# Kernel optimization log

Measured on AMD Instinct MI355X. Metric: run time of the kernel, lower is better.

The kernel has to match this reference:

```python
import jax, jax.numpy as jnp
import numpy as np

N_NODES = 50000
N_EDGES = 400000
EMB_DIM = 256
N_LAYERS = 5
MAX_NODES = 50          # nodes per graph (equal-size graphs)
N_GRAPHS = N_NODES // MAX_NODES
BN_EPS = 1e-5


def setup_inputs() -> dict:
    key = jax.random.key(0)
    ks = jax.random.split(key, 12)
    D = EMB_DIM
    x = jax.random.normal(ks[0], (N_NODES, D), dtype=jnp.float32)
    edge_index = jax.random.randint(ks[1], (2, N_EDGES), 0, N_NODES, dtype=jnp.int64)
    edge_attr = jax.random.randint(ks[2], (N_EDGES, 2), 0, 3, dtype=jnp.int64)
    batch = (jnp.arange(N_NODES, dtype=jnp.int64) // MAX_NODES)
    # per-layer parameters, stacked on leading layer axis
    s1 = 1.0 / np.sqrt(D)
    s2 = 1.0 / np.sqrt(2 * D)
    W1 = jax.random.uniform(ks[3], (N_LAYERS, D, 2 * D), jnp.float32, -s1, s1)
    b1 = jax.random.uniform(ks[4], (N_LAYERS, 2 * D), jnp.float32, -s1, s1)
    W2 = jax.random.uniform(ks[5], (N_LAYERS, 2 * D, D), jnp.float32, -s2, s2)
    b2 = jax.random.uniform(ks[6], (N_LAYERS, D), jnp.float32, -s2, s2)
    # xavier_uniform for edge embeddings
    g1 = np.sqrt(6.0 / (6 + D))
    g2 = np.sqrt(6.0 / (3 + D))
    E1 = jax.random.uniform(ks[7], (N_LAYERS, 6, D), jnp.float32, -g1, g1)
    E2 = jax.random.uniform(ks[8], (N_LAYERS, 3, D), jnp.float32, -g2, g2)
    gamma = jnp.ones((N_LAYERS, D), jnp.float32)
    beta = jnp.zeros((N_LAYERS, D), jnp.float32)
    return {"x": x, "edge_index": edge_index, "edge_attr": edge_attr,
            "batch": batch, "W1": W1, "b1": b1, "W2": W2, "b2": b2,
            "E1": E1, "E2": E2, "gamma": gamma, "beta": beta}


def reference(x, edge_index, edge_attr, batch, W1, b1, W2, b2, E1, E2, gamma, beta):
    N, D = x.shape
    # add self loops once (edge_index/edge_attr are identical every layer);
    # self-loop edge_attr fill_value = 0
    loop = jnp.arange(N, dtype=edge_index.dtype)
    src = jnp.concatenate([edge_index[0], loop])
    dst = jnp.concatenate([edge_index[1], loop])
    ea0 = jnp.concatenate([edge_attr[:, 0], jnp.zeros((N,), edge_attr.dtype)])
    ea1 = jnp.concatenate([edge_attr[:, 1], jnp.zeros((N,), edge_attr.dtype)])

    h = x
    L = W1.shape[0]
    for l in range(L):
        # GINConv: message = x_j + edge_embedding, aggr='add', update = MLP
        eemb = E1[l][ea0] + E2[l][ea1]                       # [E+N, D]
        msg = h[src] + eemb                                   # gather + add
        agg = jax.ops.segment_sum(msg, dst, num_segments=N)   # scatter-add
        h = jnp.maximum(agg @ W1[l] + b1[l], 0.0) @ W2[l] + b2[l]
        # BatchNorm1d (training mode: batch statistics over nodes)
        mu = h.mean(axis=0)
        var = h.var(axis=0)
        h = (h - mu) / jnp.sqrt(var + BN_EPS) * gamma[l] + beta[l]
        if l < L - 1:
            h = jnp.maximum(h, 0.0)  # relu (dropout p=0 is identity)

    # pad_sequence over graphs: scatter node reps into [G, MAX_NODES, D]
    G = N // MAX_NODES
    ones = jnp.ones((N,), jnp.int32)
    counts = jax.ops.segment_sum(ones, batch, num_segments=G)
    starts = jnp.cumsum(counts) - counts
    pos = jnp.arange(N) - starts[batch]
    padded = jnp.zeros((G, MAX_NODES, D), h.dtype).at[batch, pos].set(h)
    return padded
```

## Files before the change

kernel.cpp:

```cpp
#include <hip/hip_runtime.h>

#define NN 50000
#define NE 400000
#define DIM 256
#define HID 512
#define NL 5
#define BN_EPS 1e-5f
#define NB_SCAN 196

typedef float float4v __attribute__((ext_vector_type(4)));
typedef _Float16 half8 __attribute__((ext_vector_type(8)));
typedef _Float16 half4v __attribute__((ext_vector_type(4)));

__device__ __forceinline__ void gl_lds16(const void* g, void* l) {
    __builtin_amdgcn_global_load_lds((__attribute__((address_space(1))) void*)g,
                                     (__attribute__((address_space(3))) void*)l, 16, 0, 0);
}


__global__ void k_zero(int* p, int n) {
    int i = blockIdx.x * blockDim.x + threadIdx.x;
    if (i < n) p[i] = 0;
}

__global__ void k_x2h(const float* __restrict__ x, _Float16* __restrict__ xh) {
    int i = blockIdx.x * blockDim.x + threadIdx.x;
    if (i >= NN * DIM / 4) return;
    float4 v = ((const float4*)x)[i];
    half4v o;
    o.x = (_Float16)v.x; o.y = (_Float16)v.y; o.z = (_Float16)v.z; o.w = (_Float16)v.w;
    ((half4v*)xh)[i] = o;
}

__global__ void k_ctab(const float* __restrict__ E1, const float* __restrict__ E2,
                       float* __restrict__ C) {
    int b = blockIdx.x;
    int l = b / 9, ab = b % 9;
    int a = ab / 3, bb = ab % 3;
    int c = threadIdx.x;
    C[(size_t)b * DIM + c] = E1[(size_t)(l * 6 + a) * DIM + c] + E2[(size_t)(l * 3 + bb) * DIM + c];
}

__global__ void k_hist(const int* __restrict__ ei, int* __restrict__ counts) {
    int e = blockIdx.x * blockDim.x + threadIdx.x;
    if (e < NE) atomicAdd(&counts[ei[NE + e]], 1);
}

__global__ void k_bsum(const int* __restrict__ counts, int* __restrict__ bsum) {
    __shared__ int s[256];
    int t = threadIdx.x;
    int i = blockIdx.x * 256 + t;
    s[t] = (i < NN) ? counts[i] : 0;
    __syncthreads();
    for (int off = 128; off > 0; off >>= 1) {
        if (t < off) s[t] += s[t + off];
        __syncthreads();
    }
    if (t == 0) bsum[blockIdx.x] = s[0];
}

__global__ void k_bscan(const int* __restrict__ bsum, int* __restrict__ bofs) {
    __shared__ int s[256];
    int t = threadIdx.x;
    int v = (t < NB_SCAN) ? bsum[t] : 0;
    s[t] = v;
    __syncthreads();
    for (int off = 1; off < 256; off <<= 1) {
        int u = (t >= off) ? s[t - off] : 0;
        __syncthreads();
        s[t] += u;
        __syncthreads();
    }
    if (t < NB_SCAN) bofs[t] = s[t] - v;
}

__global__ void k_scatterptr(const int* __restrict__ counts, const int* __restrict__ bofs,
                             int* __restrict__ row_ptr, int* __restrict__ cursor) {
    __shared__ int s[256];
    int t = threadIdx.x;
    int i = blockIdx.x * 256 + t;
    int v = (i < NN) ? counts[i] : 0;
    s[t] = v;
    __syncthreads();
    for (int off = 1; off < 256; off <<= 1) {
        int u = (t >= off) ? s[t - off] : 0;
        __syncthreads();
        s[t] += u;
        __syncthreads();
    }
    if (i < NN) {
        int ex = bofs[blockIdx.x] + s[t] - v;
        row_ptr[i] = ex;
        cursor[i] = ex;
    }
    if (i == NN - 1) row_ptr[NN] = NE;
}

__global__ void k_fill(const int* __restrict__ ei, const int* __restrict__ ea,
                       int* __restrict__ cursor, int* __restrict__ recs) {
    int e = blockIdx.x * blockDim.x + threadIdx.x;
    if (e >= NE) return;
    int src = ei[e];
    int dst = ei[NE + e];
    int a = ea[2 * e];
    int b = ea[2 * e + 1];
    int rec = src | ((a * 3 + b) << 20);
    int pos = atomicAdd(&cursor[dst], 1);
    recs[pos] = rec;
}

__global__ void k_wt(const float* __restrict__ W, _Float16* __restrict__ T, int K, int N) {
    __shared__ float t[32][33];
    int l = blockIdx.z;
    int k0 = blockIdx.y * 32, n0 = blockIdx.x * 32;
    int tx = threadIdx.x, ty = threadIdx.y;
    const float* Wl = W + (size_t)l * K * N;
    _Float16* Tl = T + (size_t)l * N * K;
    for (int d = 0; d < 32; d += 8)
        t[ty + d][tx] = Wl[(size_t)(k0 + ty + d) * N + n0 + tx];
    __syncthreads();
    for (int d = 0; d < 32; d += 8)
        Tl[(size_t)(n0 + ty + d) * K + k0 + tx] = (_Float16)t[tx][ty + d];
}

template <bool APPLY>
__global__ __launch_bounds__(256) void k_agg(const _Float16* __restrict__ rows,
                                             const float* __restrict__ ss,
                                             const float* __restrict__ Cl,
                                             const int* __restrict__ row_ptr,
                                             const int* __restrict__ recs,
                                             _Float16* __restrict__ aggh) {
    int node = (blockIdx.x * blockDim.x + threadIdx.x) >> 6;
    int lane = threadIdx.x & 63;
    if (node >= NN) return;
    int c = lane * 4;
    float s0 = 1.f, s1 = 1.f, s2 = 1.f, s3 = 1.f, t0 = 0.f, t1 = 0.f, t2 = 0.f, t3 = 0.f;
    if (APPLY) {
        s0 = ss[c]; s1 = ss[c + 1]; s2 = ss[c + 2]; s3 = ss[c + 3];
        t0 = ss[DIM + c]; t1 = ss[DIM + c + 1]; t2 = ss[DIM + c + 2]; t3 = ss[DIM + c + 3];
    }
    float4 cv0 = *(const float4*)(Cl + c);
    half4v sv = *(const half4v*)(rows + (size_t)node * DIM + c);
    float ax, ay, az, aw;
    if (APPLY) {
        ax = fmaxf((float)sv.x * s0 + t0, 0.f) + cv0.x;
        ay = fmaxf((float)sv.y * s1 + t1, 0.f) + cv0.y;
        az = fmaxf((float)sv.z * s2 + t2, 0.f) + cv0.z;
        aw = fmaxf((float)sv.w * s3 + t3, 0.f) + cv0.w;
    } else {
        ax = (float)sv.x + cv0.x;
        ay = (float)sv.y + cv0.y;
        az = (float)sv.z + cv0.z;
        aw = (float)sv.w + cv0.w;
    }
    int e0 = row_ptr[node], e1 = row_ptr[node + 1];
    for (int e = e0; e < e1; ++e) {
        int rec = recs[e];
        int src = rec & 0xFFFFF;
        int attr = rec >> 20;
        half4v hv = *(const half4v*)(rows + (size_t)src * DIM + c);
        float4 cv = *(const float4*)(Cl + (size_t)attr * DIM + c);
        if (APPLY) {
            ax += fmaxf((float)hv.x * s0 + t0, 0.f) + cv.x;
            ay += fmaxf((float)hv.y * s1 + t1, 0.f) + cv.y;
            az += fmaxf((float)hv.z * s2 + t2, 0.f) + cv.z;
            aw += fmaxf((float)hv.w * s3 + t3, 0.f) + cv.w;
        } else {
            ax += (float)hv.x + cv.x;
            ay += (float)hv.y + cv.y;
            az += (float)hv.z + cv.z;
            aw += (float)hv.w + cv.w;
        }
    }
    half4v o;
    o.x = (_Float16)ax; o.y = (_Float16)ay; o.z = (_Float16)az; o.w = (_Float16)aw;
    *(half4v*)(aggh + (size_t)node * DIM + c) = o;
}

__global__ __launch_bounds__(256, 2) void k_mlp(const _Float16* __restrict__ A,
                                                const _Float16* __restrict__ W1t,
                                                const float* __restrict__ b1,
                                                const _Float16* __restrict__ W2t,
                                                const float* __restrict__ b2,
                                                _Float16* __restrict__ Z,
                                                float* __restrict__ stats, int M) {
    __shared__ _Float16 ldsA[64 * 128];
    __shared__ _Float16 ldsH[64 * 512];
    int tid = threadIdx.x;
    int w = tid >> 6, lane = tid & 63;
    int lm = lane & 15, lg = lane >> 4;
    int row0 = blockIdx.x * 64;

    float4v acc1[4][8];
    const float4v zero = {0.f, 0.f, 0.f, 0.f};
#pragma unroll
    for (int i = 0; i < 4; ++i)
#pragma unroll
        for (int j = 0; j < 8; ++j) acc1[i][j] = zero;

#pragma unroll
    for (int kc = 0; kc < 2; ++kc) {
        {
            int srow = lane >> 4;
            int slot = lane & 15;
#pragma unroll
            for (int j = 0; j < 4; ++j) {
                int cr = w * 16 + j * 4 + srow;
                int gr = min(row0 + cr, M - 1);
                int gk = kc * 128 + ((slot ^ (cr & 7)) * 8);
                gl_lds16(A + (size_t)gr * DIM + gk, ldsA + (w * 16 + j * 4) * 128);
            }
        }
        __syncthreads();
#pragma unroll
        for (int qq = 0; qq < 4; ++qq) {
            half8 bf[8];
#pragma unroll
            for (int nt = 0; nt < 8; ++nt) {
                int n = w * 128 + nt * 16 + lm;
                bf[nt] = *(const half8*)(W1t + (size_t)n * DIM + kc * 128 + qq * 32 + lg * 8);
            }
            half8 af[4];
#pragma unroll
            for (int mt = 0; mt < 4; ++mt) {
                int m = mt * 16 + lm;
                int slot = qq * 4 + lg;
                af[mt] = *(const half8*)(ldsA + m * 128 + ((slot ^ (m & 7)) * 8));
            }
#pragma unroll
            for (int mt = 0; mt < 4; ++mt)
#pragma unroll
                for (int nt = 0; nt < 8; ++nt)
                    acc1[mt][nt] = __builtin_amdgcn_mfma_f32_16x16x32_f16(af[mt], bf[nt],
                                                                          acc1[mt][nt], 0, 0, 0);
        }
        __syncthreads();
    }

#pragma unroll
    for (int nt = 0; nt < 8; ++nt) {
        int col = w * 128 + nt * 16 + lm;
        float bv = b1[col];
        int cs = col >> 3, ci = col & 7;
#pragma unroll
        for (int mt = 0; mt < 4; ++mt)
#pragma unroll
            for (int r = 0; r < 4; ++r) {
                int row = mt * 16 + lg * 4 + r;
                float v = fmaxf(acc1[mt][nt][r] + bv, 0.f);
                ldsH[row * 512 + ((cs ^ (row & 7)) << 3) + ci] = (_Float16)v;
            }
    }
    __syncthreads();

    float4v acc2[4][4];
#pragma unroll
    for (int i = 0; i < 4; ++i)
#pragma unroll
        for (int j = 0; j < 4; ++j) acc2[i][j] = zero;

#pragma unroll
    for (int q = 0; q < 16; ++q) {
        half8 bf[4];
#pragma unroll
        for (int nt = 0; nt < 4; ++nt) {
            int n = w * 64 + nt * 16 + lm;
            bf[nt] = *(const half8*)(W2t + (size_t)n * HID + q * 32 + lg * 8);
        }
        half8 af[4];
#pragma unroll
        for (int mt = 0; mt < 4; ++mt) {
            int m = mt * 16 + lm;
            int slot = q * 4 + lg;
            af[mt] = *(const half8*)(ldsH + m * 512 + ((slot ^ (m & 7)) << 3));
        }
#pragma unroll
        for (int mt = 0; mt < 4; ++mt)
#pragma unroll
            for (int nt = 0; nt < 4; ++nt)
                acc2[mt][nt] = __builtin_amdgcn_mfma_f32_16x16x32_f16(af[mt], bf[nt],
                                                                      acc2[mt][nt], 0, 0, 0);
    }
    __syncthreads();

    _Float16* ldsZ = ldsH;
    float psum[4], psq[4];
#pragma unroll
    for (int nt = 0; nt < 4; ++nt) { psum[nt] = 0.f; psq[nt] = 0.f; }
#pragma unroll
    for (int nt = 0; nt < 4; ++nt) {
        int col = w * 64 + nt * 16 + lm;
        float bv = b2[col];
        int cs = col >> 3, ci = col & 7;
#pragma unroll
        for (int mt = 0; mt < 4; ++mt)
#pragma unroll
            for (int r = 0; r < 4; ++r) {
                int row = mt * 16 + lg * 4 + r;
                float v = acc2[mt][nt][r] + bv;
                if (row0 + row < M) {
                    psum[nt] += v;
                    psq[nt] += v * v;
                }
                ldsZ[row * 256 + ((cs ^ (row & 7)) << 3) + ci] = (_Float16)v;
            }
    }
#pragma unroll
    for (int nt = 0; nt < 4; ++nt) {
        psum[nt] += __shfl_xor(psum[nt], 16);
        psum[nt] += __shfl_xor(psum[nt], 32);
        psq[nt] += __shfl_xor(psq[nt], 16);
        psq[nt] += __shfl_xor(psq[nt], 32);
    }
    if (lg == 0) {
#pragma unroll
        for (int nt = 0; nt < 4; ++nt) {
            int ch = w * 64 + nt * 16 + lm;
            atomicAdd(&stats[ch], psum[nt]);
            atomicAdd(&stats[DIM + ch], psq[nt]);
        }
    }
    __syncthreads();
#pragma unroll
    for (int i = 0; i < 8; ++i) {
        int s = i * 256 + tid;
        int row = s >> 5, c16 = s & 31;
        if (row0 + row < M) {
            half8 v = *(const half8*)(ldsZ + row * 256 + ((c16 ^ (row & 7)) << 3));
            *(half8*)(Z + (size_t)(row0 + row) * DIM + c16 * 8) = v;
        }
    }
}

__global__ void k_bnfin(float* __restrict__ stats, const float* __restrict__ gamma,
                        const float* __restrict__ beta, float* __restrict__ ss) {
    int c = threadIdx.x;
    float mu = stats[c] * (1.0f / NN);
    float var = stats[DIM + c] * (1.0f / NN) - mu * mu;
    float sc = gamma[c] / sqrtf(var + BN_EPS);
    ss[c] = sc;
    ss[DIM + c] = beta[c] - mu * sc;
    stats[c] = 0.f;
    stats[DIM + c] = 0.f;
}

__global__ void k_out(const _Float16* __restrict__ z, const float* __restrict__ ss,
                      float* __restrict__ out) {
    int i = blockIdx.x * blockDim.x + threadIdx.x;
    if (i >= NN * DIM / 4) return;
    int c4 = (i & (DIM / 4 - 1)) * 4;
    half4v v = ((const half4v*)z)[i];
    float4 o;
    o.x = (float)v.x * ss[c4] + ss[DIM + c4];
    o.y = (float)v.y * ss[c4 + 1] + ss[DIM + c4 + 1];
    o.z = (float)v.z * ss[c4 + 2] + ss[DIM + c4 + 2];
    o.w = (float)v.w * ss[c4 + 3] + ss[DIM + c4 + 3];
    ((float4*)out)[i] = o;
}

extern "C" void kernel_launch(void* const* d_in, const int* in_sizes, int n_in,
                              void* d_out, int out_size, void* d_ws, size_t ws_size,
                              hipStream_t stream) {
    const float* x = (const float*)d_in[0];
    const int* ei = (const int*)d_in[1];
    const int* ea = (const int*)d_in[2];
    const float* W1 = (const float*)d_in[4];
    const float* b1 = (const float*)d_in[5];
    const float* W2 = (const float*)d_in[6];
    const float* b2 = (const float*)d_in[7];
    const float* E1 = (const float*)d_in[8];
    const float* E2 = (const float*)d_in[9];
    const float* gamma = (const float*)d_in[10];
    const float* beta = (const float*)d_in[11];
    float* out = (float*)d_out;

    char* w = (char*)d_ws;
    _Float16* xh = (_Float16*)w;   w += (size_t)NN * DIM * 2;
    _Float16* z = (_Float16*)w;    w += (size_t)NN * DIM * 2;
    _Float16* aggh = (_Float16*)w; w += (size_t)NN * DIM * 2;
    _Float16* W1t = (_Float16*)w;  w += (size_t)NL * DIM * HID * 2;
    _Float16* W2t = (_Float16*)w;  w += (size_t)NL * HID * DIM * 2;
    float* Ctab = (float*)w;       w += (size_t)NL * 9 * DIM * 4;
    float* stats = (float*)w;      w += 2 * DIM * 4;
    float* ss = (float*)w;         w += 2 * DIM * 4;
    int* row_ptr = (int*)w;        w += (size_t)(NN + 2) * 4;
    int* counts = (int*)w;         w += (size_t)NN * 4;
    int* cursor = (int*)w;         w += (size_t)NN * 4;
    int* bsum = (int*)w;           w += 256 * 4;
    int* bofs = (int*)w;           w += 256 * 4;
    int* recs = (int*)w;           w += (size_t)NE * 4;

    k_zero<<<(NN + 255) / 256, 256, 0, stream>>>(counts, NN);
    k_zero<<<2, 256, 0, stream>>>((int*)stats, 2 * DIM);
    k_x2h<<<(NN * DIM / 4 + 255) / 256, 256, 0, stream>>>(x, xh);
    k_ctab<<<NL * 9, 256, 0, stream>>>(E1, E2, Ctab);
    k_hist<<<(NE + 255) / 256, 256, 0, stream>>>(ei, counts);
    k_bsum<<<NB_SCAN, 256, 0, stream>>>(counts, bsum);
    k_bscan<<<1, 256, 0, stream>>>(bsum, bofs);
    k_scatterptr<<<NB_SCAN, 256, 0, stream>>>(counts, bofs, row_ptr, cursor);
    k_fill<<<(NE + 255) / 256, 256, 0, stream>>>(ei, ea, cursor, recs);
    {
        dim3 b(32, 8);
        dim3 g1(HID / 32, DIM / 32, NL);
        k_wt<<<g1, b, 0, stream>>>(W1, W1t, DIM, HID);
        dim3 g2(DIM / 32, HID / 32, NL);
        k_wt<<<g2, b, 0, stream>>>(W2, W2t, HID, DIM);
    }

    for (int l = 0; l < NL; ++l) {
        const float* Cl = Ctab + (size_t)l * 9 * DIM;
        if (l == 0)
            k_agg<false><<<(NN + 3) / 4, 256, 0, stream>>>(xh, ss, Cl, row_ptr, recs, aggh);
        else
            k_agg<true><<<(NN + 3) / 4, 256, 0, stream>>>(z, ss, Cl, row_ptr, recs, aggh);

        k_mlp<<<(NN + 63) / 64, 256, 0, stream>>>(aggh, W1t + (size_t)l * DIM * HID,
                                                  b1 + (size_t)l * HID,
                                                  W2t + (size_t)l * HID * DIM,
                                                  b2 + (size_t)l * DIM, z, stats, NN);

        k_bnfin<<<1, 256, 0, stream>>>(stats, gamma + (size_t)l * DIM, beta + (size_t)l * DIM, ss);
    }
    k_out<<<(NN * DIM / 4 + 255) / 256, 256, 0, stream>>>(z, ss, out);
}
```

Measured before the change: 878.6 us.

## Chunk MLP hidden dimension to cut LDS and registers, raise occupancy

The fused two-layer MLP kernel now computes the 512-wide hidden layer in four 128-column chunks. Each chunk is fed straight into the second GEMM instead of materialising the full hidden tile. This cuts the hidden LDS buffer from 64x512 to 64x128 and the first-layer accumulators from 32 to 8 per wave, so launch bounds are raised to 3 blocks per CU. The full 64x256 input tile is loaded once up front. In exchange it needs more barriers per block, and the second GEMM must reload the W2 weights across chunks.

```diff
diff --git a/kernel.cpp b/kernel.cpp
--- a/kernel.cpp
+++ b/kernel.cpp
@@ -177,113 +177,111 @@
     *(half4v*)(aggh + (size_t)node * DIM + c) = o;
 }
 
-__global__ __launch_bounds__(256, 2) void k_mlp(const _Float16* __restrict__ A,
+__global__ __launch_bounds__(256, 3) void k_mlp(const _Float16* __restrict__ A,
                                                 const _Float16* __restrict__ W1t,
                                                 const float* __restrict__ b1,
                                                 const _Float16* __restrict__ W2t,
                                                 const float* __restrict__ b2,
                                                 _Float16* __restrict__ Z,
                                                 float* __restrict__ stats, int M) {
-    __shared__ _Float16 ldsA[64 * 128];
-    __shared__ _Float16 ldsH[64 * 512];
+    __shared__ _Float16 ldsA[64 * 256];
+    __shared__ _Float16 ldsH[64 * 128];
     int tid = threadIdx.x;
     int w = tid >> 6, lane = tid & 63;
     int lm = lane & 15, lg = lane >> 4;
     int row0 = blockIdx.x * 64;
 
-    float4v acc1[4][8];
+#pragma unroll
+    for (int i = 0; i < 8; ++i) {
+        int t = w * 512 + i * 64 + lane;
+        int m = t >> 5;
+        int p = t & 31;
+        int s = p ^ (m & 7);
+        int gr = min(row0 + m, M - 1);
+        gl_lds16(A + (size_t)gr * DIM + s * 8, ldsA + (w * 16 + i * 2) * 256);
+    }
+    __syncthreads();
+
     const float4v zero = {0.f, 0.f, 0.f, 0.f};
+    float4v acc2[4][4];
 #pragma unroll
     for (int i = 0; i < 4; ++i)
 #pragma unroll
-        for (int j = 0; j < 8; ++j) acc1[i][j] = zero;
-
-#pragma unroll
-    for (int kc = 0; kc < 2; ++kc) {
-        {
-            int srow = lane >> 4;
-            int slot = lane & 15;
-#pragma unroll
-            for (int j = 0; j < 4; ++j) {
-                int cr = w * 16 + j * 4 + srow;
-                int gr = min(row0 + cr, M - 1);
-                int gk = kc * 128 + ((slot ^ (cr & 7)) * 8);
-                gl_lds16(A + (size_t)gr * DIM + gk, ldsA + (w * 16 + j * 4) * 128);
-            }
-        }
-        __syncthreads();
-#pragma unroll
-        for (int qq = 0; qq < 4; ++qq) {
-            half8 bf[8];
-#pragma unroll
-            for (int nt = 0; nt < 8; ++nt) {
-                int n = w * 128 + nt * 16 + lm;
-                bf[nt] = *(const half8*)(W1t + (size_t)n * DIM + kc * 128 + qq * 32 + lg * 8);
+        for (int j = 0; j < 4; ++j) acc2[i][j] = zero;
+
+#pragma unroll
+    for (int qt = 0; qt < 4; ++qt) {
+        float4v acc1[4][2];
+#pragma unroll
+        for (int i = 0; i < 4; ++i)
+#pragma unroll
+            for (int j = 0; j < 2; ++j) acc1[i][j] = zero;
+
+#pragma unroll
+        for (int q = 0; q < 8; ++q) {
+            half8 bf[2];
+#pragma unroll
+            for (int nt = 0; nt < 2; ++nt) {
+                int n = qt * 128 + w * 32 + nt * 16 + lm;
+                bf[nt] = *(const half8*)(W1t + (size_t)n * DIM + q * 32 + lg * 8);
             }
             half8 af[4];
 #pragma unroll
             for (int mt = 0; mt < 4; ++mt) {
                 int m = mt * 16 + lm;
-                int slot = qq * 4 + lg;
-                af[mt] = *(const half8*)(ldsA + m * 128 + ((slot ^ (m & 7)) * 8));
+                int sl = q * 4 + lg;
+                af[mt] = *(const half8*)(ldsA + m * 256 + ((sl ^ (m & 7)) * 8));
             }
 #pragma unroll
             for (int mt = 0; mt < 4; ++mt)
 #pragma unroll
-                for (int nt = 0; nt < 8; ++nt)
+                for (int nt = 0; nt < 2; ++nt)
                     acc1[mt][nt] = __builtin_amdgcn_mfma_f32_16x16x32_f16(af[mt], bf[nt],
                                                                           acc1[mt][nt], 0, 0, 0);
         }
-        __syncthreads();
-    }
-
-#pragma unroll
-    for (int nt = 0; nt < 8; ++nt) {
-        int col = w * 128 + nt * 16 + lm;
-        float bv = b1[col];
-        int cs = col >> 3, ci = col & 7;
-#pragma unroll
-        for (int mt = 0; mt < 4; ++mt)
-#pragma unroll
-            for (int r = 0; r < 4; ++r) {
-                int row = mt * 16 + lg * 4 + r;
-                float v = fmaxf(acc1[mt][nt][r] + bv, 0.f);
-                ldsH[row * 512 + ((cs ^ (row & 7)) << 3) + ci] = (_Float16)v;
+
+#pragma unroll
+        for (int nt = 0; nt < 2; ++nt) {
+            int cq = w * 32 + nt * 16 + lm;
+            float bv = b1[qt * 128 + cq];
+            int cs = cq >> 3, ci = cq & 7;
+#pragma unroll
+            for (int mt = 0; mt < 4; ++mt)
+#pragma unroll
+                for (int r = 0; r < 4; ++r) {
+                    int row = mt * 16 + lg * 4 + r;
+                    float v = fmaxf(acc1[mt][nt][r] + bv, 0.f);
+                    ldsH[row * 128 + ((cs ^ (row & 7)) << 3) + ci] = (_Float16)v;
+                }
+        }
+        __syncthreads();
+
+#pragma unroll
+        for (int qloc = 0; qloc < 4; ++qloc) {
+            half8 bf2[4];
+#pragma unroll
+            for (int nt = 0; nt < 4; ++nt) {
+                int n = w * 64 + nt * 16 + lm;
+                bf2[nt] = *(const half8*)(W2t + (size_t)n * HID + qt * 128 + qloc * 32 + lg * 8);
             }
-    }
-    __syncthreads();
-
-    float4v acc2[4][4];
-#pragma unroll
-    for (int i = 0; i < 4; ++i)
-#pragma unroll
-        for (int j = 0; j < 4; ++j) acc2[i][j] = zero;
-
-#pragma unroll
-    for (int q = 0; q < 16; ++q) {
-        half8 bf[4];
-#pragma unroll
-        for (int nt = 0; nt < 4; ++nt) {
-            int n = w * 64 + nt * 16 + lm;
-            bf[nt] = *(const half8*)(W2t + (size_t)n * HID + q * 32 + lg * 8);
-        }
-        half8 af[4];
-#pragma unroll
-        for (int mt = 0; mt < 4; ++mt) {
-            int m = mt * 16 + lm;
-            int slot = q * 4 + lg;
-            af[mt] = *(const half8*)(ldsH + m * 512 + ((slot ^ (m & 7)) << 3));
-        }
-#pragma unroll
-        for (int mt = 0; mt < 4; ++mt)
-#pragma unroll
-            for (int nt = 0; nt < 4; ++nt)
-                acc2[mt][nt] = __builtin_amdgcn_mfma_f32_16x16x32_f16(af[mt], bf[nt],
-                                                                      acc2[mt][nt], 0, 0, 0);
-    }
-    __syncthreads();
-
-    _Float16* ldsZ = ldsH;
+            half8 af[4];
+#pragma unroll
+            for (int mt = 0; mt < 4; ++mt) {
+                int m = mt * 16 + lm;
+                int sl = qloc * 4 + lg;
+                af[mt] = *(const half8*)(ldsH + m * 128 + ((sl ^ (m & 7)) << 3));
+            }
+#pragma unroll
+            for (int mt = 0; mt < 4; ++mt)
+#pragma unroll
+                for (int nt = 0; nt < 4; ++nt)
+                    acc2[mt][nt] = __builtin_amdgcn_mfma_f32_16x16x32_f16(af[mt], bf2[nt],
+                                                                          acc2[mt][nt], 0, 0, 0);
+        }
+        __syncthreads();
+    }
+
+    _Float16* ldsZ = ldsA;
     float psum[4], psq[4];
 #pragma unroll
     for (int nt = 0; nt < 4; ++nt) { psum[nt] = 0.f; psq[nt] = 0.f; }
```

After: 1.069 ms. +21.6%, slower.
